# Performance work log

Measured on AMD Instinct MI355X. Metric: run time of the kernel, lower is better.

## Reference

```python
import jax, jax.numpy as jnp
import numpy as np
from jax import lax

MAX_OBJ = 100
IOU_THRES = 0.45
SCORE_THRES = 0.25
MAX_WH = 7680.0

# xywh -> xyxy conversion matrix (same as ONNX_ORT.convert_matrix)
CONVERT = jnp.array([[1, 0, 1, 0],
                     [0, 1, 0, 1],
                     [-0.5, 0, 0.5, 0],
                     [0, -0.5, 0, 0.5]], dtype=jnp.float32)


def _iou_one_vs_all(box, boxes):
    # box: [4] xyxy, boxes: [N,4] xyxy
    x1 = jnp.maximum(box[0], boxes[:, 0])
    y1 = jnp.maximum(box[1], boxes[:, 1])
    x2 = jnp.minimum(box[2], boxes[:, 2])
    y2 = jnp.minimum(box[3], boxes[:, 3])
    inter = jnp.clip(x2 - x1, 0.0) * jnp.clip(y2 - y1, 0.0)
    a = (box[2] - box[0]) * (box[3] - box[1])
    b = (boxes[:, 2] - boxes[:, 0]) * (boxes[:, 3] - boxes[:, 1])
    return inter / (a + b - inter + 1e-9)


def _nms_indices(nmsbox, max_score):
    # Greedy class-offset NMS; returns [MAX_OBJ] indices, -1 for padding.
    valid0 = max_score >= SCORE_THRES

    def step(valid, _):
        s = jnp.where(valid, max_score, -1.0)
        i = jnp.argmax(s)
        ok = s[i] >= SCORE_THRES
        iou = _iou_one_vs_all(nmsbox[i], nmsbox)
        valid = valid & (iou <= IOU_THRES)
        valid = valid.at[i].set(False)
        return valid, jnp.where(ok, i, -1)

    _, idxs = lax.scan(step, valid0, None, length=MAX_OBJ)
    return idxs


def _forward(x1, x2, num_labels1, num_labels2):
    B, N1, _ = x1.shape
    N2 = x2.shape[1]
    # pad x1 class scores with zeros for model2's labels (appended at end)
    x1p = jnp.concatenate([x1, jnp.zeros((B, N1, num_labels2), x1.dtype)], axis=2)
    # pad x2: insert zeros for model1's labels between conf and its own classes
    x2p = jnp.concatenate([x2[:, :, 0:5],
                           jnp.zeros((B, N2, num_labels1), x2.dtype),
                           x2[:, :, 5:]], axis=2)
    x = jnp.concatenate([x1p, x2p], axis=1)  # [B, N1+N2, 5+C1+C2]

    boxes = x[:, :, :4] @ CONVERT            # xywh -> xyxy, [B,N,4]
    conf = x[:, :, 4:5]
    scores = x[:, :, 5:] * conf              # [B,N,C]
    max_score = scores.max(axis=2)           # [B,N]
    cat_id = scores.argmax(axis=2)           # [B,N]
    # class-offset boxes so NMS is class-aware
    nmsbox = boxes + cat_id[..., None].astype(boxes.dtype) * MAX_WH

    idxs = jax.vmap(_nms_indices)(lax.stop_gradient(nmsbox),
                                  lax.stop_gradient(max_score))  # [B,MAX_OBJ]
    mask = idxs >= 0
    si = jnp.maximum(idxs, 0)
    sel_boxes = jnp.take_along_axis(boxes, si[..., None], axis=1)      # [B,MAX_OBJ,4]
    sel_cat = jnp.take_along_axis(cat_id, si, axis=1).astype(boxes.dtype)
    sel_score = jnp.take_along_axis(max_score, si, axis=1)

    mf = mask.astype(boxes.dtype)
    Xcol = jnp.where(mask, jnp.arange(B)[:, None], -1).astype(boxes.dtype)
    out = jnp.concatenate([Xcol[..., None],
                           sel_boxes * mf[..., None],
                           (sel_cat * mf)[..., None],
                           (sel_score * mf)[..., None]], axis=2)
    return out.reshape(B * MAX_OBJ, 7)


def setup_inputs() -> dict:
    key = jax.random.key(0)
    k1, k2 = jax.random.split(key)
    x1 = jax.random.uniform(k1, (4, 25200, 85), dtype=jnp.float32)
    x2 = jax.random.uniform(k2, (4, 25200, 25), dtype=jnp.float32)
    return {"x1": x1, "x2": x2, "num_labels1": 80, "num_labels2": 20}


def reference(x1, x2, num_labels1, num_labels2):
    return _forward(x1, x2, num_labels1, num_labels2)
```

## Files before the change

kernel.cpp:

```cpp
#include <hip/hip_runtime.h>
#include <stdint.h>

#pragma clang fp contract(off)

#define BATCH 4
#define N1 25200
#define NROW 50400
#define NCLS 100
#define TOT (BATCH*NROW)
#define CAPB 2048
#define SCORE_T 0.25f
#define IOU_T 0.45f
#define MAXWH 7680.0f

#define X1_SLAB 64
#define X1_SPB 394
#define X2_SLAB 256
#define X2_SPB 99

typedef unsigned long long u64;

__device__ __forceinline__ u64 pack_key(unsigned sb, int n, int cid) {
    return ((u64)sb << 32) | ((u64)(unsigned)((n ^ 0xFFFF) & 0xFFFF) << 8) | (u64)(unsigned)cid;
}

__global__ __launch_bounds__(256) void k_rows(const float* __restrict__ x1,
                                              const float* __restrict__ x2,
                                              float4* __restrict__ boxes4,
                                              u64* __restrict__ rowKey) {
    __shared__ float4 ld4[1600];
    float* ld = (float*)ld4;
    int blk = blockIdx.x;
    int t = threadIdx.x;
    const int NX1 = BATCH * X1_SPB;
    if (blk < NX1) {
        int b = blk / X1_SPB, s = blk - b * X1_SPB;
        int r0 = s * X1_SLAB;
        int nr = min(X1_SLAB, N1 - r0);
        const float4* src = (const float4*)(x1 + ((size_t)b * N1 + r0) * 85);
        int count4 = (nr * 85) >> 2;
        for (int i = t; i < count4; i += 256) ld4[i] = src[i];
        __syncthreads();
        int row = t >> 2, sub = t & 3;
        if (row < nr) {
            const float* p = ld + row * 85;
            float conf = p[4];
            u64 key = 0ULL;
            int base = sub * 20;
            for (int c = 0; c < 20; ++c) {
                int j = base + c;
                float v = p[5 + j] * conf;
                u64 kk = ((u64)__float_as_uint(v) << 32) | (unsigned)~(unsigned)j;
                if (kk > key) key = kk;
            }
            u64 o;
            o = __shfl_xor(key, 1, 64); if (o > key) key = o;
            o = __shfl_xor(key, 2, 64); if (o > key) key = o;
            if (sub == 0) {
                float best = __uint_as_float((unsigned)(key >> 32));
                int bestj = ~(unsigned)key;
                int n = r0 + row;
                int r = b * NROW + n;
                u64 outk = 0ULL;
                if (best >= SCORE_T) {
                    float cx = p[0], cy = p[1], w = p[2], h = p[3];
                    boxes4[r] = make_float4(cx - 0.5f * w, cy - 0.5f * h,
                                            cx + 0.5f * w, cy + 0.5f * h);
                    outk = pack_key((unsigned)(key >> 32), n, bestj);
                }
                rowKey[r] = outk;
            }
        }
    } else {
        int blk2 = blk - NX1;
        int b = blk2 / X2_SPB, s = blk2 - b * X2_SPB;
        int r0 = s * X2_SLAB;
        int nr = min(X2_SLAB, N1 - r0);
        const float4* src = (const float4*)(x2 + ((size_t)b * N1 + r0) * 25);
        int count4 = (nr * 25) >> 2;
        for (int i = t; i < count4; i += 256) ld4[i] = src[i];
        __syncthreads();
        if (t < nr) {
            const float* p = ld + t * 25;
            float conf = p[4];
            float best = 0.0f; int bestj = 0;
            for (int j2 = 0; j2 < 20; ++j2) {
                float v = p[5 + j2] * conf;
                if (v > best) { best = v; bestj = 80 + j2; }
            }
            int n = N1 + r0 + t;
            int r = b * NROW + n;
            u64 outk = 0ULL;
            if (best >= SCORE_T) {
                float cx = p[0], cy = p[1], w = p[2], h = p[3];
                boxes4[r] = make_float4(cx - 0.5f * w, cy - 0.5f * h,
                                        cx + 0.5f * w, cy + 0.5f * h);
                outk = pack_key(__float_as_uint(best), n, bestj);
            }
            rowKey[r] = outk;
        }
    }
}

__global__ __launch_bounds__(256) void k_nms(const float4* __restrict__ boxes4,
                                             const u64* __restrict__ rowKey,
                                             u64* __restrict__ accKey,
                                             int* __restrict__ accCnt) {
    __shared__ u64 sk[CAPB];
    __shared__ float4 cQ[CAPB];
    __shared__ float4 accQ[100];
    __shared__ int wcnt[4];
    int blk = blockIdx.x;
    int b, c;
    if (blk < BATCH * 20) { b = blk / 20; c = 80 + (blk - b * 20); }
    else { int z = blk - BATCH * 20; b = z / 80; c = z - b * 80; }
    int bucket = b * NCLS + c;
    int t = threadIdx.x;
    int lane = t & 63, wid = t >> 6;

    int rowBase = (c >= 80) ? N1 : 0;
    const ulonglong2* rk2 = (const ulonglong2*)(rowKey + (size_t)b * NROW + rowBase);
    const int SLICE = 3150;
    u64* temp = ((u64*)cQ) + wid * 512;
    int wbase = 0;
    for (int i = wid * SLICE + lane; i < (wid + 1) * SLICE; i += 64) {
        ulonglong2 kk = rk2[i];
        bool m0 = (kk.x != 0ULL) && ((int)(kk.x & 0xFF) == c);
        bool m1 = (kk.y != 0ULL) && ((int)(kk.y & 0xFF) == c);
        u64 mb0 = __ballot(m0), mb1 = __ballot(m1);
        u64 below = (1ULL << lane) - 1ULL;
        if (m0) { int p = wbase + __popcll(mb0 & below); if (p < 512) temp[p] = kk.x; }
        if (m1) { int p = wbase + __popcll(mb0) + __popcll(mb1 & below); if (p < 512) temp[p] = kk.y; }
        wbase += __popcll(mb0) + __popcll(mb1);
    }
    if (lane == 0) wcnt[wid] = min(wbase, 512);
    __syncthreads();
    int w0 = wcnt[0], w1 = wcnt[1], w2 = wcnt[2], w3 = wcnt[3];
    int cnt0 = w0 + w1 + w2 + w3;
    if (cnt0 == 0) { if (t == 0) accCnt[bucket] = 0; return; }
    int myoff = (wid > 0 ? w0 : 0) + (wid > 1 ? w1 : 0) + (wid > 2 ? w2 : 0);
    int mycnt = wcnt[wid];
    for (int i = lane; i < mycnt; i += 64) sk[myoff + i] = temp[i];
    int L = 512; while (L < cnt0) L <<= 1;
    for (int i = cnt0 + t; i < L; i += 256) sk[i] = 0ULL;
    __syncthreads();

    bool act = (t * 8) < L;
    u64 r[8];
    if (act) {
#pragma unroll
        for (int e = 0; e < 8; ++e) r[e] = sk[t * 8 + e];
    }
    for (int k = 2; k <= L; k <<= 1) {
        for (int j = k >> 1; j > 0; j >>= 1) {
            if (j >= 512) {
                if (act) {
#pragma unroll
                    for (int e = 0; e < 8; ++e) sk[t * 8 + e] = r[e];
                }
                __syncthreads();
                if (act) {
                    bool iAmLo = (t & (j >> 3)) == 0;
                    bool descSeg = (t & (k >> 3)) == 0;
                    bool takeMax = (descSeg == iAmLo);
#pragma unroll
                    for (int e = 0; e < 8; ++e) {
                        u64 u = r[e];
                        u64 v = sk[(t * 8 + e) ^ j];
                        bool uGE = (u >= v);
                        r[e] = (takeMax == uGE) ? u : v;
                    }
                }
                __syncthreads();
            } else if (j >= 8) {
                if (act) {
                    int dt = j >> 3;
                    bool iAmLo = (t & dt) == 0;
                    bool descSeg = (t & (k >> 3)) == 0;
                    bool takeMax = (descSeg == iAmLo);
#pragma unroll
                    for (int e = 0; e < 8; ++e) {
                        u64 u = r[e];
                        u64 v = __shfl_xor(u, dt, 64);
                        bool uGE = (u >= v);
                        r[e] = (takeMax == uGE) ? u : v;
                    }
                }
            } else {
                if (act) {
#pragma unroll
                    for (int e = 0; e < 8; ++e) {
                        if (!(e & j)) {
                            int e2 = e | j;
                            bool descSeg = (k >= 8) ? ((t & (k >> 3)) == 0)
                                                    : ((e & k) == 0);
                            u64 lo = r[e], hi = r[e2];
                            bool sw = descSeg ? (lo < hi) : (lo > hi);
                            if (sw) { r[e] = hi; r[e2] = lo; }
                        }
                    }
                }
            }
        }
    }
    if (act) {
#pragma unroll
        for (int e = 0; e < 8; ++e) sk[t * 8 + e] = r[e];
    }
    __syncthreads();

    float off = (float)c * MAXWH;
    for (int i = t; i < cnt0; i += 256) {
        u64 k = sk[i];
        int n = 0xFFFF ^ (int)((k >> 8) & 0xFFFF);
        float4 v = boxes4[b * NROW + n];
        v.x += off; v.y += off; v.z += off; v.w += off;
        cQ[i] = v;
    }
    __syncthreads();

    if (t >= 64) return;
    int m = 0;
    for (int base = 0; base < cnt0 && m < 100; base += 64) {
        int j = base + lane;
        bool alive = (j < cnt0);
        float4 a = make_float4(0.f, 0.f, 0.f, 0.f);
        float aA = 0.f; u64 myKey = 0ULL;
        if (alive) { a = cQ[j]; myKey = sk[j]; aA = (a.z - a.x) * (a.w - a.y); }
        int k2 = 0;
        while (k2 < m) {
            if (__ballot(alive) == 0ULL) break;
            int lim = min(k2 + 8, m);
            for (; k2 < lim; ++k2) {
                float4 q = accQ[k2];
                float qa = (q.z - q.x) * (q.w - q.y);
                float xx1 = fmaxf(a.x, q.x), yy1 = fmaxf(a.y, q.y);
                float xx2 = fminf(a.z, q.z), yy2 = fminf(a.w, q.w);
                float inter = fmaxf(xx2 - xx1, 0.f) * fmaxf(yy2 - yy1, 0.f);
                if (inter / (qa + aA - inter + 1e-9f) > IOU_T) alive = false;
            }
        }
        u64 av = __ballot(alive);
        while (av != 0ULL && m < 100) {
            int f = __builtin_ctzll(av);
            float qx = __shfl(a.x, f, 64), qy = __shfl(a.y, f, 64);
            float qz = __shfl(a.z, f, 64), qw = __shfl(a.w, f, 64);
            if (lane == f) {
                accQ[m] = a;
                accKey[(size_t)bucket * 100 + m] = myKey;
                alive = false;
            }
            ++m;
            if (alive) {
                float qa = (qz - qx) * (qw - qy);
                float xx1 = fmaxf(a.x, qx), yy1 = fmaxf(a.y, qy);
                float xx2 = fminf(a.z, qz), yy2 = fminf(a.w, qw);
                float inter = fmaxf(xx2 - xx1, 0.f) * fmaxf(yy2 - yy1, 0.f);
                if (inter / (qa + aA - inter + 1e-9f) > IOU_T) alive = false;
            }
            av = __ballot(alive);
        }
    }
    if (lane == 0) accCnt[bucket] = m;
}

__global__ __launch_bounds__(256) void k_merge(const float4* __restrict__ boxes4,
                                               const u64* __restrict__ accKey,
                                               const int* __restrict__ accCnt,
                                               float* __restrict__ out) {
    __shared__ u64 keys[NCLS * 100];
    __shared__ u64 winKey[100];
    __shared__ int cnts[NCLS];
    int b = blockIdx.x;
    int t = threadIdx.x;
    if (t < NCLS) cnts[t] = accCnt[b * NCLS + t];
    __syncthreads();
    for (int i = t; i < NCLS * 100; i += 256) {
        int c = i / 100, j = i - c * 100;
        keys[i] = (j < cnts[c]) ? accKey[(size_t)(b * NCLS + c) * 100 + j] : 0ULL;
    }
    __syncthreads();
    if (t < 64) {
        int c0 = 2 * t, c1 = 2 * t + 1;
        int h0 = 0, h1 = 0;
        u64 hk0 = (c0 < NCLS && cnts[c0] > 0) ? keys[c0 * 100] : 0ULL;
        u64 hk1 = (c1 < NCLS && cnts[c1] > 0) ? keys[c1 * 100] : 0ULL;
        for (int step = 0; step < 100; ++step) {
            u64 k = (hk0 >= hk1) ? hk0 : hk1;
            for (int o = 1; o < 64; o <<= 1) {
                u64 ok = __shfl_xor(k, o, 64);
                if (ok > k) k = ok;
            }
            if (t == 0) winKey[step] = k;
            if (k != 0ULL) {
                int cls = (int)(k & 0xFF);
                if (cls == c0)      { ++h0; hk0 = (h0 < cnts[c0]) ? keys[c0 * 100 + h0] : 0ULL; }
                else if (cls == c1) { ++h1; hk1 = (h1 < cnts[c1]) ? keys[c1 * 100 + h1] : 0ULL; }
            }
        }
    }
    __syncthreads();
    if (t < 100) {
        u64 k = winKey[t];
        float* o7 = out + (size_t)(b * 100 + t) * 7;
        if (k == 0ULL) {
            o7[0] = -1.0f;
            o7[1] = 0.0f; o7[2] = 0.0f; o7[3] = 0.0f;
            o7[4] = 0.0f; o7[5] = 0.0f; o7[6] = 0.0f;
        } else {
            int n = 0xFFFF ^ (int)((k >> 8) & 0xFFFF);
            int cid = (int)(k & 0xFF);
            float4 bx = boxes4[b * NROW + n];
            o7[0] = (float)b;
            o7[1] = bx.x; o7[2] = bx.y; o7[3] = bx.z; o7[4] = bx.w;
            o7[5] = (float)cid;
            o7[6] = __uint_as_float((unsigned)(k >> 32));
        }
    }
}

extern "C" void kernel_launch(void* const* d_in, const int* in_sizes, int n_in,
                              void* d_out, int out_size, void* d_ws, size_t ws_size,
                              hipStream_t stream) {
    const float* x1 = (const float*)d_in[0];
    const float* x2 = (const float*)d_in[1];
    float* out = (float*)d_out;

    float4* boxes4 = (float4*)d_ws;
    u64* rowKey = (u64*)(boxes4 + TOT);
    u64* accKey = rowKey + TOT;
    int* accCnt = (int*)(accKey + (size_t)BATCH * NCLS * 100);

    int rowBlocks = BATCH * X1_SPB + BATCH * X2_SPB;
    k_rows<<<rowBlocks, 256, 0, stream>>>(x1, x2, boxes4, rowKey);
    k_nms<<<BATCH * NCLS, 256, 0, stream>>>(boxes4, rowKey, accKey, accCnt);
    k_merge<<<BATCH, 256, 0, stream>>>(boxes4, accKey, accCnt, out);
}
```

Baseline: 160.9 us.

## Run per-class greedy NMS with all four waves and division-free IoU test

The per-bucket NMS phase used to run on a single 64-lane wave. Now each chunk of 256 candidates is first filtered in parallel by all four waves against the boxes already kept. The waves then take turns, one after another, to catch up on boxes kept during this chunk and to append their own survivors. Kept-box areas are cached in shared memory, register broadcasts use readlane instead of shfl, and the IoU threshold is checked with a multiply-compare that falls back to exact division only near the boundary. The price is extra block barriers and the serial turn-taking across waves.

```diff
diff --git a/kernel.cpp b/kernel.cpp
--- a/kernel.cpp
+++ b/kernel.cpp
@@ -22,6 +22,18 @@
 
 __device__ __forceinline__ u64 pack_key(unsigned sb, int n, int cid) {
     return ((u64)sb << 32) | ((u64)(unsigned)((n ^ 0xFFFF) & 0xFFFF) << 8) | (u64)(unsigned)cid;
+}
+
+__device__ __forceinline__ bool sup_test(float inter, float sum) {
+    float d = (sum - inter) + 1e-9f;
+    float t1 = IOU_T * d;
+    if (inter > t1 * 1.00001f) return true;
+    if (inter < t1 * 0.99999f) return false;
+    return (inter / d) > IOU_T;
+}
+
+__device__ __forceinline__ float rl(float v, int srcLane) {
+    return __int_as_float(__builtin_amdgcn_readlane(__float_as_int(v), srcLane));
 }
 
 __global__ __launch_bounds__(256) void k_rows(const float* __restrict__ x1,
@@ -109,7 +121,9 @@
     __shared__ u64 sk[CAPB];
     __shared__ float4 cQ[CAPB];
     __shared__ float4 accQ[100];
+    __shared__ float accA[100];
     __shared__ int wcnt[4];
+    __shared__ int mSh;
     int blk = blockIdx.x;
     int b, c;
     if (blk < BATCH * 20) { b = blk / 20; c = 80 + (blk - b * 20); }
@@ -217,51 +231,70 @@
         v.x += off; v.y += off; v.z += off; v.w += off;
         cQ[i] = v;
     }
-    __syncthreads();
-
-    if (t >= 64) return;
-    int m = 0;
-    for (int base = 0; base < cnt0 && m < 100; base += 64) {
-        int j = base + lane;
+    if (t == 0) mSh = 0;
+    __syncthreads();
+
+    for (int base = 0; base < cnt0; base += 256) {
+        int m0 = mSh;
+        if (m0 >= 100) break;
+        int j = base + t;
         bool alive = (j < cnt0);
         float4 a = make_float4(0.f, 0.f, 0.f, 0.f);
         float aA = 0.f; u64 myKey = 0ULL;
         if (alive) { a = cQ[j]; myKey = sk[j]; aA = (a.z - a.x) * (a.w - a.y); }
         int k2 = 0;
-        while (k2 < m) {
+        while (k2 < m0) {
             if (__ballot(alive) == 0ULL) break;
-            int lim = min(k2 + 8, m);
+            int lim = min(k2 + 8, m0);
             for (; k2 < lim; ++k2) {
                 float4 q = accQ[k2];
-                float qa = (q.z - q.x) * (q.w - q.y);
+                float qa = accA[k2];
                 float xx1 = fmaxf(a.x, q.x), yy1 = fmaxf(a.y, q.y);
                 float xx2 = fminf(a.z, q.z), yy2 = fminf(a.w, q.w);
                 float inter = fmaxf(xx2 - xx1, 0.f) * fmaxf(yy2 - yy1, 0.f);
-                if (inter / (qa + aA - inter + 1e-9f) > IOU_T) alive = false;
-            }
-        }
-        u64 av = __ballot(alive);
-        while (av != 0ULL && m < 100) {
-            int f = __builtin_ctzll(av);
-            float qx = __shfl(a.x, f, 64), qy = __shfl(a.y, f, 64);
-            float qz = __shfl(a.z, f, 64), qw = __shfl(a.w, f, 64);
-            if (lane == f) {
-                accQ[m] = a;
-                accKey[(size_t)bucket * 100 + m] = myKey;
-                alive = false;
-            }
-            ++m;
-            if (alive) {
-                float qa = (qz - qx) * (qw - qy);
-                float xx1 = fmaxf(a.x, qx), yy1 = fmaxf(a.y, qy);
-                float xx2 = fminf(a.z, qz), yy2 = fminf(a.w, qw);
-                float inter = fmaxf(xx2 - xx1, 0.f) * fmaxf(yy2 - yy1, 0.f);
-                if (inter / (qa + aA - inter + 1e-9f) > IOU_T) alive = false;
-            }
-            av = __ballot(alive);
-        }
-    }
-    if (lane == 0) accCnt[bucket] = m;
+                if (sup_test(inter, qa + aA)) alive = false;
+            }
+        }
+        __syncthreads();
+        for (int w = 0; w < 4; ++w) {
+            if (wid == w) {
+                int mNow = mSh;
+                for (int k2d = m0; k2d < mNow; ++k2d) {
+                    if (__ballot(alive) == 0ULL) break;
+                    float4 q = accQ[k2d];
+                    float qa = accA[k2d];
+                    float xx1 = fmaxf(a.x, q.x), yy1 = fmaxf(a.y, q.y);
+                    float xx2 = fminf(a.z, q.z), yy2 = fminf(a.w, q.w);
+                    float inter = fmaxf(xx2 - xx1, 0.f) * fmaxf(yy2 - yy1, 0.f);
+                    if (sup_test(inter, qa + aA)) alive = false;
+                }
+                u64 av = __ballot(alive);
+                int m = mNow;
+                while (av != 0ULL && m < 100) {
+                    int f = __builtin_ctzll(av);
+                    float qx = rl(a.x, f), qy = rl(a.y, f);
+                    float qz = rl(a.z, f), qw = rl(a.w, f);
+                    float qa = rl(aA, f);
+                    if (lane == f) {
+                        accQ[m] = a; accA[m] = aA;
+                        accKey[(size_t)bucket * 100 + m] = myKey;
+                        alive = false;
+                    }
+                    ++m;
+                    if (alive) {
+                        float xx1 = fmaxf(a.x, qx), yy1 = fmaxf(a.y, qy);
+                        float xx2 = fminf(a.z, qz), yy2 = fminf(a.w, qw);
+                        float inter = fmaxf(xx2 - xx1, 0.f) * fmaxf(yy2 - yy1, 0.f);
+                        if (sup_test(inter, qa + aA)) alive = false;
+                    }
+                    av = __ballot(alive);
+                }
+                if (lane == 0) mSh = m;
+            }
+            __syncthreads();
+        }
+    }
+    if (t == 0) accCnt[bucket] = mSh;
 }
 
 __global__ __launch_bounds__(256) void k_merge(const float4* __restrict__ boxes4,
```

Result: slower. 179.6 us (+11.6%).

## Split NMS into sort-prep and single-wave greedy kernels with division-free IoU test

Applied to the files above, without the earlier changes.

The fused per-bucket NMS kernel is split into a 256-thread prep kernel (filter and bitonic sort, writing up to 1152 sorted keys per bucket to global memory) and a 64-thread greedy kernel that gathers boxes directly from global memory. This drops the large shared-memory box queue so both kernels can run at higher occupancy, and keeps the three idle waves from holding resources during the serial greedy phase. The IoU threshold check now multiplies instead of dividing and falls back to an exact division only near the boundary. Kept-box areas are cached, and readlane replaces shfl for broadcasting. The costs are an extra launch and a global round trip of the sorted keys. The 1152 cap truncates candidates per bucket, which is a correctness risk if a bucket needs more than that.

```diff
diff --git a/kernel.cpp b/kernel.cpp
--- a/kernel.cpp
+++ b/kernel.cpp
@@ -9,6 +9,7 @@
 #define NCLS 100
 #define TOT (BATCH*NROW)
 #define CAPB 2048
+#define CAPG 1152
 #define SCORE_T 0.25f
 #define IOU_T 0.45f
 #define MAXWH 7680.0f
@@ -22,6 +23,24 @@
 
 __device__ __forceinline__ u64 pack_key(unsigned sb, int n, int cid) {
     return ((u64)sb << 32) | ((u64)(unsigned)((n ^ 0xFFFF) & 0xFFFF) << 8) | (u64)(unsigned)cid;
+}
+
+__device__ __forceinline__ bool sup_test(float inter, float sum) {
+    float d = (sum - inter) + 1e-9f;
+    float t1 = IOU_T * d;
+    bool hi = inter > t1 * 1.00001f;
+    bool lo = inter < t1 * 0.99999f;
+    if (__builtin_expect(!(hi || lo), 0)) return (inter / d) > IOU_T;
+    return hi;
+}
+
+__device__ __forceinline__ float rl(float v, int srcLane) {
+    return __int_as_float(__builtin_amdgcn_readlane(__float_as_int(v), srcLane));
+}
+
+__device__ __forceinline__ void blk2bucket(int blk, int& b, int& c) {
+    if (blk < BATCH * 20) { b = blk / 20; c = 80 + (blk - b * 20); }
+    else { int z = blk - BATCH * 20; b = z / 80; c = z - b * 80; }
 }
 
 __global__ __launch_bounds__(256) void k_rows(const float* __restrict__ x1,
@@ -102,18 +121,13 @@
     }
 }
 
-__global__ __launch_bounds__(256) void k_nms(const float4* __restrict__ boxes4,
-                                             const u64* __restrict__ rowKey,
-                                             u64* __restrict__ accKey,
-                                             int* __restrict__ accCnt) {
+__global__ __launch_bounds__(256) void k_prep(const u64* __restrict__ rowKey,
+                                              u64* __restrict__ skG,
+                                              int* __restrict__ cntArr) {
     __shared__ u64 sk[CAPB];
-    __shared__ float4 cQ[CAPB];
-    __shared__ float4 accQ[100];
+    __shared__ u64 temp2[2048];
     __shared__ int wcnt[4];
-    int blk = blockIdx.x;
-    int b, c;
-    if (blk < BATCH * 20) { b = blk / 20; c = 80 + (blk - b * 20); }
-    else { int z = blk - BATCH * 20; b = z / 80; c = z - b * 80; }
+    int b, c; blk2bucket(blockIdx.x, b, c);
     int bucket = b * NCLS + c;
     int t = threadIdx.x;
     int lane = t & 63, wid = t >> 6;
@@ -121,7 +135,7 @@
     int rowBase = (c >= 80) ? N1 : 0;
     const ulonglong2* rk2 = (const ulonglong2*)(rowKey + (size_t)b * NROW + rowBase);
     const int SLICE = 3150;
-    u64* temp = ((u64*)cQ) + wid * 512;
+    u64* temp = temp2 + wid * 512;
     int wbase = 0;
     for (int i = wid * SLICE + lane; i < (wid + 1) * SLICE; i += 64) {
         ulonglong2 kk = rk2[i];
@@ -137,7 +151,7 @@
     __syncthreads();
     int w0 = wcnt[0], w1 = wcnt[1], w2 = wcnt[2], w3 = wcnt[3];
     int cnt0 = w0 + w1 + w2 + w3;
-    if (cnt0 == 0) { if (t == 0) accCnt[bucket] = 0; return; }
+    if (cnt0 == 0) { if (t == 0) cntArr[bucket] = 0; return; }
     int myoff = (wid > 0 ? w0 : 0) + (wid > 1 ? w1 : 0) + (wid > 2 ? w2 : 0);
     int mycnt = wcnt[wid];
     for (int i = lane; i < mycnt; i += 64) sk[myoff + i] = temp[i];
@@ -209,54 +223,82 @@
     }
     __syncthreads();
 
+    int cw = min(cnt0, CAPG);
+    for (int i = t; i < cw; i += 256) skG[(size_t)bucket * CAPG + i] = sk[i];
+    if (t == 0) cntArr[bucket] = cw;
+}
+
+__global__ __launch_bounds__(64) void k_greedy(const float4* __restrict__ boxes4,
+                                               const u64* __restrict__ skG,
+                                               const int* __restrict__ cntArr,
+                                               u64* __restrict__ accKey,
+                                               int* __restrict__ accCnt) {
+    __shared__ float4 accQ[100];
+    __shared__ float accA[100];
+    int b, c; blk2bucket(blockIdx.x, b, c);
+    int bucket = b * NCLS + c;
+    int lane = threadIdx.x;
+    int cnt0 = cntArr[bucket];
+    if (cnt0 == 0) { if (lane == 0) accCnt[bucket] = 0; return; }
+    const u64* skB = skG + (size_t)bucket * CAPG;
     float off = (float)c * MAXWH;
-    for (int i = t; i < cnt0; i += 256) {
-        u64 k = sk[i];
-        int n = 0xFFFF ^ (int)((k >> 8) & 0xFFFF);
-        float4 v = boxes4[b * NROW + n];
-        v.x += off; v.y += off; v.z += off; v.w += off;
-        cQ[i] = v;
-    }
-    __syncthreads();
-
-    if (t >= 64) return;
     int m = 0;
     for (int base = 0; base < cnt0 && m < 100; base += 64) {
         int j = base + lane;
         bool alive = (j < cnt0);
         float4 a = make_float4(0.f, 0.f, 0.f, 0.f);
         float aA = 0.f; u64 myKey = 0ULL;
-        if (alive) { a = cQ[j]; myKey = sk[j]; aA = (a.z - a.x) * (a.w - a.y); }
+        if (alive) {
+            myKey = skB[j];
+            int n = 0xFFFF ^ (int)((myKey >> 8) & 0xFFFF);
+            a = boxes4[b * NROW + n];
+            a.x += off; a.y += off; a.z += off; a.w += off;
+            aA = (a.z - a.x) * (a.w - a.y);
+        }
         int k2 = 0;
         while (k2 < m) {
             if (__ballot(alive) == 0ULL) break;
-            int lim = min(k2 + 8, m);
-            for (; k2 < lim; ++k2) {
-                float4 q = accQ[k2];
-                float qa = (q.z - q.x) * (q.w - q.y);
-                float xx1 = fmaxf(a.x, q.x), yy1 = fmaxf(a.y, q.y);
-                float xx2 = fminf(a.z, q.z), yy2 = fminf(a.w, q.w);
-                float inter = fmaxf(xx2 - xx1, 0.f) * fmaxf(yy2 - yy1, 0.f);
-                if (inter / (qa + aA - inter + 1e-9f) > IOU_T) alive = false;
+            int rem = m - k2;
+            if (rem >= 8) {
+#pragma unroll
+                for (int u = 0; u < 8; ++u) {
+                    float4 q = accQ[k2 + u];
+                    float qa = accA[k2 + u];
+                    float xx1 = fmaxf(a.x, q.x), yy1 = fmaxf(a.y, q.y);
+                    float xx2 = fminf(a.z, q.z), yy2 = fminf(a.w, q.w);
+                    float inter = fmaxf(xx2 - xx1, 0.f) * fmaxf(yy2 - yy1, 0.f);
+                    alive = alive && !sup_test(inter, qa + aA);
+                }
+                k2 += 8;
+            } else {
+                for (int u = 0; u < rem; ++u) {
+                    float4 q = accQ[k2 + u];
+                    float qa = accA[k2 + u];
+                    float xx1 = fmaxf(a.x, q.x), yy1 = fmaxf(a.y, q.y);
+                    float xx2 = fminf(a.z, q.z), yy2 = fminf(a.w, q.w);
+                    float inter = fmaxf(xx2 - xx1, 0.f) * fmaxf(yy2 - yy1, 0.f);
+                    alive = alive && !sup_test(inter, qa + aA);
+                }
+                k2 = m;
             }
         }
         u64 av = __ballot(alive);
         while (av != 0ULL && m < 100) {
             int f = __builtin_ctzll(av);
-            float qx = __shfl(a.x, f, 64), qy = __shfl(a.y, f, 64);
-            float qz = __shfl(a.z, f, 64), qw = __shfl(a.w, f, 64);
+            float qx = rl(a.x, f), qy = rl(a.y, f);
+            float qz = rl(a.z, f), qw = rl(a.w, f);
+            float qa = rl(aA, f);
             if (lane == f) {
-                accQ[m] = a;
+                accQ[m] = a; accA[m] = aA;
                 accKey[(size_t)bucket * 100 + m] = myKey;
                 alive = false;
             }
             ++m;
             if (alive) {
-                float qa = (qz - qx) * (qw - qy);
                 float xx1 = fmaxf(a.x, qx), yy1 = fmaxf(a.y, qy);
                 float xx2 = fminf(a.z, qz), yy2 = fminf(a.w, qw);
                 float inter = fmaxf(xx2 - xx1, 0.f) * fmaxf(yy2 - yy1, 0.f);
-                if (inter / (qa + aA - inter + 1e-9f) > IOU_T) alive = false;
+                alive = !sup_test(inter, qa + aA);
             }
             av = __ballot(alive);
         }
@@ -328,11 +370,14 @@
 
     float4* boxes4 = (float4*)d_ws;
     u64* rowKey = (u64*)(boxes4 + TOT);
-    u64* accKey = rowKey + TOT;
-    int* accCnt = (int*)(accKey + (size_t)BATCH * NCLS * 100);
+    u64* skG    = rowKey + TOT;
+    u64* accKey = skG + (size_t)BATCH * NCLS * CAPG;
+    int* cntArr = (int*)(accKey + (size_t)BATCH * NCLS * 100);
+    int* accCnt = cntArr + BATCH * NCLS;
 
     int rowBlocks = BATCH * X1_SPB + BATCH * X2_SPB;
     k_rows<<<rowBlocks, 256, 0, stream>>>(x1, x2, boxes4, rowKey);
-    k_nms<<<BATCH * NCLS, 256, 0, stream>>>(boxes4, rowKey, accKey, accCnt);
+    k_prep<<<BATCH * NCLS, 256, 0, stream>>>(rowKey, skG, cntArr);
+    k_greedy<<<BATCH * NCLS, 64, 0, stream>>>(boxes4, skG, cntArr, accKey, accCnt);
     k_merge<<<BATCH, 256, 0, stream>>>(boxes4, accKey, accCnt, out);
 }
```

After: 166.1 us. 1.03x slower.
